# Kernel optimization log

Measured on AMD Instinct MI355X. Metric: run time of the kernel, lower is better.

## Reference

```python
import jax, jax.numpy as jnp
import numpy as np

B, H, S, DK = 2, 16, 2048, 64


def setup_inputs() -> dict:
    key = jax.random.key(0)
    k1, k2, k3, k4 = jax.random.split(key, 4)
    Q = jax.random.normal(k1, (B, H, S, DK), dtype=jnp.float32)
    K = jax.random.normal(k2, (B, H, S, DK), dtype=jnp.float32)
    V = jax.random.normal(k3, (B, H, S, DK), dtype=jnp.float32)
    attn_mask = jax.random.randint(k4, (B, 1, S, S), 0, 2).astype(jnp.bool_)
    return {"Q": Q, "K": K, "V": V, "attn_mask": attn_mask}


def reference(Q, K, V, attn_mask):
    d_k = Q.shape[-1]
    scale = 1.0 / jnp.sqrt(jnp.asarray(d_k, dtype=Q.dtype))
    # scores: [B,H,S,S]
    scores = jnp.einsum('bhqd,bhkd->bhqk', Q, K) * scale
    scores = jnp.where(attn_mask, jnp.asarray(-1e9, dtype=scores.dtype), scores)
    attn = jax.nn.softmax(scores, axis=-1)
    # dropout in eval mode (identity) for deterministic reference
    return jnp.einsum('bhqk,bhkd->bhqd', attn, V)
```

## Files before the change

### kernel.cpp

```cpp
#include <hip/hip_runtime.h>
#include <hip/hip_bf16.h>

#define Bdim 2
#define Hdim 16
#define Sdim 2048
#define Ddim 64
#define NT2 64
#define WQ 32
#define NWAVE 4
#define QTILE (WQ * NWAVE)
#define QSCL (0.125f * 1.44269504088896f)
#define SCALE 0.125f
#define WREG 8192

typedef __bf16 bf16x8 __attribute__((ext_vector_type(8)));
typedef float  f32x4  __attribute__((ext_vector_type(4)));
typedef float  f32x16 __attribute__((ext_vector_type(16)));
typedef unsigned u32x4 __attribute__((ext_vector_type(4)));

__device__ __forceinline__ void gll16(const __bf16* g, __bf16* l) {
  __builtin_amdgcn_global_load_lds(
      (const __attribute__((address_space(1))) void*)g,
      (__attribute__((address_space(3))) void*)l, 16, 0, 0);
}
__device__ __forceinline__ unsigned cvtpk_raw(float lo, float hi) {
  unsigned r;
  asm("v_cvt_pk_bf16_f32 %0, %1, %2" : "=v"(r) : "v"(lo), "v"(hi));
  return r;
}
template <bool SW>
__device__ __forceinline__ unsigned pko(float a, float b) {
  return SW ? cvtpk_raw(b, a) : cvtpk_raw(a, b);
}
__device__ __forceinline__ unsigned cvtpk(float a, float b, bool sw) {
  const float lo = sw ? b : a;
  const float hi = sw ? a : b;
  return cvtpk_raw(lo, hi);
}
template <bool SW>
__device__ __forceinline__ void packAll32(const float (&sv)[16],
                                          unsigned (&pw)[8]) {
#pragma unroll
  for (int ks = 0; ks < 2; ++ks) {
    const int rb = 8 * ks;
    pw[ks * 4 + 0] = pko<SW>(sv[rb + 0], sv[rb + 1]);
    pw[ks * 4 + 1] = pko<SW>(sv[rb + 2], sv[rb + 3]);
    pw[ks * 4 + 2] = pko<SW>(sv[rb + 4], sv[rb + 5]);
    pw[ks * 4 + 3] = pko<SW>(sv[rb + 6], sv[rb + 7]);
  }
}

__global__ __launch_bounds__(256) void prep_all(
    const void* __restrict__ mask, unsigned long long* __restrict__ packed,
    const float* __restrict__ K, const float* __restrict__ V,
    __bf16* __restrict__ Kb, __bf16* __restrict__ Vt) {
  __shared__ __bf16 tile[64][72];
  const int t = threadIdx.x;

  if (blockIdx.x < 512) {
    const int nwords = Bdim * Sdim * (Sdim / 64);
    const unsigned* m32 = (const unsigned*)mask;
    const unsigned char* m8 = (const unsigned char*)mask;
    int gid = blockIdx.x * 256 + t;
    int lane = gid & 63;
    int wid = gid >> 6;
    const int nwaves = 512 * 256 / 64;
    bool isBytes = __any(m32[lane] > 1u);
    for (int w = wid; w < nwords; w += nwaves) {
      int v = isBytes ? (int)m8[(size_t)w * 64 + lane]
                      : (int)m32[(size_t)w * 64 + lane];
      unsigned long long bal = __ballot(v != 0);
      if (lane == 0) packed[w] = bal;
    }
    return;
  }

  const int idx = blockIdx.x - 512;
  const int bh = idx >> 5, st = idx & 31;
  const int r = t >> 2, c0 = (t & 3) << 4;
  {
    const float* ks = K + ((size_t)bh * Sdim + st * 64 + r) * Ddim + c0;
    bf16x8 o0, o1;
#pragma unroll
    for (int j = 0; j < 8; ++j) o0[j] = (__bf16)ks[j];
#pragma unroll
    for (int j = 0; j < 8; ++j) o1[j] = (__bf16)ks[8 + j];
    __bf16* kd = Kb + ((size_t)bh * Sdim + st * 64 + r) * Ddim + c0;
    *(bf16x8*)kd = o0;
    *(bf16x8*)(kd + 8) = o1;
  }
  {
    const float* vs = V + ((size_t)bh * Sdim + st * 64 + r) * Ddim + c0;
#pragma unroll
    for (int j = 0; j < 16; ++j) tile[r][c0 + j] = (__bf16)vs[j];
  }
  __syncthreads();
  {
    const int d = t >> 2, s0 = (t & 3) << 4;
    __bf16 o[16];
#pragma unroll
    for (int j = 0; j < 16; ++j) o[j] = tile[s0 + j][d];
    __bf16* dst = Vt + ((size_t)bh * Ddim + d) * Sdim + st * 64 + s0;
    *(bf16x8*)dst = *(bf16x8*)&o[0];
    *(bf16x8*)(dst + 8) = *(bf16x8*)&o[8];
  }
}

__global__ __launch_bounds__(256, 2) void attn7(
    const float* __restrict__ Q, const __bf16* __restrict__ Kb,
    const __bf16* __restrict__ Vt,
    const unsigned long long* __restrict__ maskP, float* __restrict__ Out) {
  __shared__ alignas(16) __bf16 sm[NWAVE * WREG];

  const int tid = threadIdx.x;
  const int lane = tid & 63;
  const int w = tid >> 6;
  const int l31 = lane & 31;
  const int hi = lane >> 5;

  const int bid = blockIdx.x;
  const int bh = bid & 31;
  const int qt = bid >> 5;
  const int b = bh >> 4;
  const int qrow = qt * QTILE + w * WQ + l31;

  const __bf16* Kbase = Kb + (size_t)bh * Sdim * Ddim;
  const __bf16* Vbase = Vt + (size_t)bh * (size_t)Ddim * Sdim;
  const unsigned* mp32 =
      (const unsigned*)(maskP + ((size_t)b * Sdim + qrow) * (Sdim / 64));

  __bf16* smw = sm + w * WREG;

  const bool sw = (cvtpk_raw(0.0f, 1.0f) & 0xFFFFu) != 0u;

  bf16x8 qf[4];
  {
    const float* qs = Q + ((size_t)bh * Sdim + qrow) * Ddim;
#pragma unroll
    for (int step = 0; step < 4; ++step) {
      const int d0 = step * 16 + hi * 8;
      float4 a = *(const float4*)(qs + d0);
      float4 c = *(const float4*)(qs + d0 + 4);
      u32x4 f;
      f[0] = cvtpk(a.x * QSCL, a.y * QSCL, sw);
      f[1] = cvtpk(a.z * QSCL, a.w * QSCL, sw);
      f[2] = cvtpk(c.x * QSCL, c.y * QSCL, sw);
      f[3] = cvtpk(c.z * QSCL, c.w * QSCL, sw);
      qf[step] = __builtin_bit_cast(bf16x8, f);
    }
  }

  const int lr3 = lane >> 3;
  const int ksb = (lane & 7) ^ lr3;
  const int vbp = (lane & 7) ^ lr3;
  const int vd0 = 2 * lr3 + (vbp >> 2);
  const int vsc = vbp & 3;

  const __bf16* kpS = Kbase + (size_t)lr3 * Ddim + ksb * 8;
  const __bf16* vpS = Vbase + (size_t)vd0 * Sdim + vsc * 8;

  const __bf16* kf[4];
#pragma unroll
  for (int s = 0; s < 4; ++s)
    kf[s] = smw + l31 * 64 + (((s * 2 + hi) ^ (l31 & 7)) << 3);
  const __bf16* vfp[2][2];
#pragma unroll
  for (int half = 0; half < 2; ++half)
#pragma unroll
    for (int ks = 0; ks < 2; ++ks)
      vfp[half][ks] = smw + 2048 + half * 1024 + (l31 >> 1) * 64 +
                      ((((l31 & 1) * 4 + ks * 2 + hi) ^ ((l31 >> 1) & 7)) << 3);

  f32x16 otA = {0,0,0,0,0,0,0,0,0,0,0,0,0,0,0,0};
  f32x16 otB = {0,0,0,0,0,0,0,0,0,0,0,0,0,0,0,0};
  float lrow = 0.f;

  unsigned mw32 = mp32[0];
  const unsigned* mpp = mp32 + 1;
  {
    gll16(kpS, smw);
    gll16(kpS + 8 * Ddim, smw + 512);
    gll16(kpS + 16 * Ddim, smw + 1024);
    gll16(kpS + 24 * Ddim, smw + 1536);
    gll16(vpS, smw + 2048);
    gll16(vpS + 16 * Sdim, smw + 2560);
    gll16(vpS + 32 * Sdim, smw + 3072);
    gll16(vpS + 48 * Sdim, smw + 3584);
    kpS += 32 * Ddim;
    vpS += 32;
  }

  unsigned mwNext;

#define ITER2(BUFC, STBUF, LAST)                                               \
  do {                                                                         \
    if (!(LAST)) {                                                             \
      mwNext = *mpp++;                                                         \
      gll16(kpS, smw + (STBUF));                                               \
      gll16(kpS + 8 * Ddim, smw + (STBUF) + 512);                              \
      gll16(kpS + 16 * Ddim, smw + (STBUF) + 1024);                            \
      gll16(kpS + 24 * Ddim, smw + (STBUF) + 1536);                            \
      gll16(vpS, smw + (STBUF) + 2048);                                        \
      gll16(vpS + 16 * Sdim, smw + (STBUF) + 2560);                            \
      gll16(vpS + 32 * Sdim, smw + (STBUF) + 3072);                            \
      gll16(vpS + 48 * Sdim, smw + (STBUF) + 3584);                            \
      kpS += 32 * Ddim;                                                        \
      vpS += 32;                                                               \
       \
      asm volatile("s_waitcnt vmcnt(9)" ::: "memory");                         \
    } else {                                                                   \
      asm volatile("s_waitcnt vmcnt(0)" ::: "memory");                         \
    }                                                                          \
    __builtin_amdgcn_sched_barrier(0);                                         \
    f32x16 st = {0,0,0,0,0,0,0,0,0,0,0,0,0,0,0,0};                             \
    __builtin_amdgcn_s_setprio(1);                                             \
    st = __builtin_amdgcn_mfma_f32_32x32x16_bf16(                              \
        *(const bf16x8*)(kf[0] + (BUFC)), qf[0], st, 0, 0, 0);                 \
    st = __builtin_amdgcn_mfma_f32_32x32x16_bf16(                              \
        *(const bf16x8*)(kf[1] + (BUFC)), qf[1], st, 0, 0, 0);                 \
    st = __builtin_amdgcn_mfma_f32_32x32x16_bf16(                              \
        *(const bf16x8*)(kf[2] + (BUFC)), qf[2], st, 0, 0, 0);                 \
    st = __builtin_amdgcn_mfma_f32_32x32x16_bf16(                              \
        *(const bf16x8*)(kf[3] + (BUFC)), qf[3], st, 0, 0, 0);                 \
    __builtin_amdgcn_s_setprio(0);                                             \
    float sv[16];                                                              \
    const unsigned ws_ = mw32 >> (hi * 4);                                     \
    _Pragma("unroll") for (int r = 0; r < 16; ++r) {                           \
      const int cr = (r & 3) + 8 * (r >> 2);                                   \
      const float e0 = __builtin_amdgcn_exp2f(st[r]);                          \
      sv[r] = ((ws_ >> cr) & 1u) ? 0.f : e0;                                   \
    }                                                                          \
    {                                                                          \
      float s8_[8];                                                            \
      _Pragma("unroll") for (int j = 0; j < 8; ++j) s8_[j] = sv[j] + sv[j + 8];\
      lrow += ((s8_[0] + s8_[4]) + (s8_[1] + s8_[5])) +                        \
              ((s8_[2] + s8_[6]) + (s8_[3] + s8_[7]));                         \
    }                                                                          \
    unsigned pw[8];                                                            \
    if (!sw) packAll32<false>(sv, pw);                                         \
    else     packAll32<true>(sv, pw);                                          \
    bf16x8 pb[2];                                                              \
    _Pragma("unroll") for (int ks = 0; ks < 2; ++ks) {                         \
      const unsigned W0 = pw[ks * 4 + 0], W1 = pw[ks * 4 + 1];                 \
      const unsigned X0 = pw[ks * 4 + 2], X1 = pw[ks * 4 + 3];                 \
      const unsigned s1 = hi ? W0 : X0;                                        \
      const unsigned s2 = hi ? W1 : X1;                                        \
      const unsigned r1 = __shfl_xor(s1, 32, 64);                              \
      const unsigned r2 = __shfl_xor(s2, 32, 64);                              \
      u32x4 wv;                                                                \
      wv[0] = hi ? r1 : W0;                                                    \
      wv[1] = hi ? r2 : W1;                                                    \
      wv[2] = hi ? X0 : r1;                                                    \
      wv[3] = hi ? X1 : r2;                                                    \
      pb[ks] = __builtin_bit_cast(bf16x8, wv);                                 \
    }                                                                          \
    __builtin_amdgcn_s_setprio(1);                                             \
    otA = __builtin_amdgcn_mfma_f32_32x32x16_bf16(                             \
        *(const bf16x8*)(vfp[0][0] + (BUFC)), pb[0], otA, 0, 0, 0);            \
    otA = __builtin_amdgcn_mfma_f32_32x32x16_bf16(                             \
        *(const bf16x8*)(vfp[0][1] + (BUFC)), pb[1], otA, 0, 0, 0);            \
    otB = __builtin_amdgcn_mfma_f32_32x32x16_bf16(                             \
        *(const bf16x8*)(vfp[1][0] + (BUFC)), pb[0], otB, 0, 0, 0);            \
    otB = __builtin_amdgcn_mfma_f32_32x32x16_bf16(                             \
        *(const bf16x8*)(vfp[1][1] + (BUFC)), pb[1], otB, 0, 0, 0);            \
    __builtin_amdgcn_s_setprio(0);                                             \
    mw32 = mwNext;                                                             \
  } while (0)

#pragma unroll 1
  for (int g = 0; g < 31; ++g) {
    ITER2(0, 4096, false);
    ITER2(4096, 0, false);
  }
  ITER2(0, 4096, false);
  ITER2(4096, 0, true);
#undef ITER2

  lrow += __shfl_xor(lrow, 32, 64);
  const float inv = 1.f / (lrow + 1e-30f);
  float* orow = Out + ((size_t)bh * Sdim + qrow) * Ddim;
#pragma unroll
  for (int g = 0; g < 4; ++g) {
    const int d0 = 8 * g + 4 * hi;
    float4 va = {otA[4 * g] * inv, otA[4 * g + 1] * inv,
                 otA[4 * g + 2] * inv, otA[4 * g + 3] * inv};
    float4 vb = {otB[4 * g] * inv, otB[4 * g + 1] * inv,
                 otB[4 * g + 2] * inv, otB[4 * g + 3] * inv};
    *(float4*)(orow + d0) = va;
    *(float4*)(orow + 32 + d0) = vb;
  }
}

__global__ __launch_bounds__(256) void attn_fallback(
    const float* __restrict__ Q, const float* __restrict__ K,
    const float* __restrict__ V, const void* __restrict__ maskRaw,
    float* __restrict__ Out) {
  __shared__ alignas(16) __bf16 Kl[64 * Ddim];
  __shared__ alignas(16) __bf16 Vts[Ddim * 64];
  __shared__ alignas(16) __bf16 Pl[4][16 * 64];

  const int tid = threadIdx.x;
  const int lane = tid & 63;
  const int w = tid >> 6;
  const int lhi = lane >> 4;
  const int llo = lane & 15;

  const int qt = blockIdx.x;
  const int bh = blockIdx.y;
  const int b = bh >> 4;
  const int qbase = qt * 64;

  const float* Qp = Q + (size_t)bh * Sdim * Ddim;
  const float* Kp = K + (size_t)bh * Sdim * Ddim;
  const float* Vp = V + (size_t)bh * Sdim * Ddim;

  bool maskBytes = __any(((const unsigned*)maskRaw)[lane] > 1u);

  bf16x8 qf0, qf1;
  {
    const int qr = qbase + w * 16 + llo;
    const float* src = Qp + (size_t)qr * Ddim + lhi * 8;
#pragma unroll
    for (int i = 0; i < 8; ++i) qf0[i] = (__bf16)(src[i] * SCALE);
#pragma unroll
    for (int i = 0; i < 8; ++i) qf1[i] = (__bf16)(src[32 + i] * SCALE);
  }

  f32x4 acc[4] = {{0.f,0.f,0.f,0.f},{0.f,0.f,0.f,0.f},
                  {0.f,0.f,0.f,0.f},{0.f,0.f,0.f,0.f}};
  float mrow[4], lrw[4];
#pragma unroll
  for (int r = 0; r < 4; ++r) { mrow[r] = -3.0e38f; lrw[r] = 0.f; }

  for (int kt = 0; kt < Sdim / 64; ++kt) {
    __syncthreads();
    {
      int r = tid >> 2;
      int c0 = (tid & 3) << 4;
      const float* ks = Kp + (size_t)(kt * 64 + r) * Ddim + c0;
      const float* vs = Vp + (size_t)(kt * 64 + r) * Ddim + c0;
      float kv[16], vv[16];
#pragma unroll
      for (int j = 0; j < 4; ++j) {
        *(float4*)(&kv[j * 4]) = *(const float4*)(ks + j * 4);
        *(float4*)(&vv[j * 4]) = *(const float4*)(vs + j * 4);
      }
      const int swzK = (r & 7) << 3;
      bf16x8 k0v, k1v;
#pragma unroll
      for (int j = 0; j < 8; ++j) { k0v[j] = (__bf16)kv[j]; k1v[j] = (__bf16)kv[8 + j]; }
      *(bf16x8*)&Kl[r * 64 + (c0 ^ swzK)] = k0v;
      *(bf16x8*)&Kl[r * 64 + ((c0 + 8) ^ swzK)] = k1v;
#pragma unroll
      for (int j = 0; j < 16; ++j) {
        int d = c0 + j;
        Vts[d * 64 + (r ^ ((d & 7) << 3))] = (__bf16)vv[j];
      }
    }
    __syncthreads();

    float sv[4][4];
#pragma unroll
    for (int cb = 0; cb < 4; ++cb) {
      int krow = cb * 16 + llo;
      int swz = (krow & 7) << 3;
      bf16x8 kf0 = *(const bf16x8*)&Kl[krow * 64 + ((lhi * 8) ^ swz)];
      bf16x8 kf1 = *(const bf16x8*)&Kl[krow * 64 + ((32 + lhi * 8) ^ swz)];
      f32x4 s = {0.f, 0.f, 0.f, 0.f};
      s = __builtin_amdgcn_mfma_f32_16x16x32_bf16(qf0, kf0, s, 0, 0, 0);
      s = __builtin_amdgcn_mfma_f32_16x16x32_bf16(qf1, kf1, s, 0, 0, 0);
#pragma unroll
      for (int r = 0; r < 4; ++r) {
        size_t q = qbase + w * 16 + lhi * 4 + r;
        size_t k = (size_t)kt * 64 + cb * 16 + llo;
        size_t idx = ((size_t)b * Sdim + q) * Sdim + k;
        bool masked = maskBytes ? (((const unsigned char*)maskRaw)[idx] != 0)
                                : (((const int*)maskRaw)[idx] != 0);
        sv[cb][r] = masked ? -1e9f : s[r];
      }
    }

    float corr[4], tsum[4];
#pragma unroll
    for (int r = 0; r < 4; ++r) {
      float mx = fmaxf(fmaxf(sv[0][r], sv[1][r]), fmaxf(sv[2][r], sv[3][r]));
#pragma unroll
      for (int off = 1; off < 16; off <<= 1)
        mx = fmaxf(mx, __shfl_xor(mx, off, 64));
      float mnew = fmaxf(mrow[r], mx);
      corr[r] = __expf(mrow[r] - mnew);
      mrow[r] = mnew;
      tsum[r] = 0.f;
    }
#pragma unroll
    for (int cb = 0; cb < 4; ++cb) {
#pragma unroll
      for (int r = 0; r < 4; ++r) {
        float p = __expf(sv[cb][r] - mrow[r]);
        tsum[r] += p;
        int row = lhi * 4 + r;
        int col = cb * 16 + llo;
        Pl[w][row * 64 + (col ^ ((row & 7) << 3))] = (__bf16)p;
      }
    }
#pragma unroll
    for (int r = 0; r < 4; ++r) {
      float s = tsum[r];
#pragma unroll
      for (int off = 1; off < 16; off <<= 1)
        s += __shfl_xor(s, off, 64);
      lrw[r] = lrw[r] * corr[r] + s;
#pragma unroll
      for (int db = 0; db < 4; ++db) acc[db][r] *= corr[r];
    }
    asm volatile("s_waitcnt lgkmcnt(0)" ::: "memory");

    bf16x8 pf0 = *(const bf16x8*)&Pl[w][llo * 64 + ((lhi * 8) ^ ((llo & 7) << 3))];
    bf16x8 pf1 = *(const bf16x8*)&Pl[w][llo * 64 + ((32 + lhi * 8) ^ ((llo & 7) << 3))];
#pragma unroll
    for (int db = 0; db < 4; ++db) {
      int d = db * 16 + llo;
      int swz = (d & 7) << 3;
      bf16x8 vf0 = *(const bf16x8*)&Vts[d * 64 + ((lhi * 8) ^ swz)];
      bf16x8 vf1 = *(const bf16x8*)&Vts[d * 64 + ((32 + lhi * 8) ^ swz)];
      acc[db] = __builtin_amdgcn_mfma_f32_16x16x32_bf16(pf0, vf0, acc[db], 0, 0, 0);
      acc[db] = __builtin_amdgcn_mfma_f32_16x16x32_bf16(pf1, vf1, acc[db], 0, 0, 0);
    }
  }

#pragma unroll
  for (int r = 0; r < 4; ++r) {
    float inv = 1.f / lrw[r];
    int q = qbase + w * 16 + lhi * 4 + r;
    float* dst = Out + ((size_t)bh * Sdim + q) * Ddim + llo;
#pragma unroll
    for (int db = 0; db < 4; ++db) dst[db * 16] = acc[db][r] * inv;
  }
}

extern "C" void kernel_launch(void* const* d_in, const int* in_sizes, int n_in,
                              void* d_out, int out_size, void* d_ws, size_t ws_size,
                              hipStream_t stream) {
  const float* Q = (const float*)d_in[0];
  const float* K = (const float*)d_in[1];
  const float* V = (const float*)d_in[2];
  const void* mask = d_in[3];
  float* out = (float*)d_out;

  const size_t packed_bytes =
      (size_t)Bdim * Sdim * (Sdim / 64) * sizeof(unsigned long long);
  const size_t tensor_bf16 = (size_t)Bdim * Hdim * Sdim * Ddim * 2;

  if (ws_size >= packed_bytes + 2 * tensor_bf16) {
    unsigned long long* packed = (unsigned long long*)d_ws;
    __bf16* Kb = (__bf16*)((char*)d_ws + packed_bytes);
    __bf16* Vt = (__bf16*)((char*)d_ws + packed_bytes + tensor_bf16);
    prep_all<<<512 + Bdim * Hdim * (Sdim / 64), 256, 0, stream>>>(
        mask, packed, K, V, Kb, Vt);
    attn7<<<(Sdim / QTILE) * Bdim * Hdim, 256, 0, stream>>>(Q, Kb, Vt, packed, out);
  } else {
    attn_fallback<<<dim3(Sdim / 64, Bdim * Hdim), 256, 0, stream>>>(Q, K, V, mask, out);
  }
}
```

Baseline: 111.3 us.

## Share K/V tiles across waves with triple-buffered LDS and two interleaved KV halves

Before, each wave loaded its own private copy of every K/V tile into LDS. Now all four waves cooperatively stage one shared K/V tile per step into a triple-buffered LDS ring, synchronised with a block barrier, which cuts global-to-LDS traffic by about four times. The key sequence is split into two halves that are processed in the same loop iteration, giving two independent QK^T/softmax/PV chains for more instruction-level parallelism. It also swaps the shuffle-based P repacking for v_permlane32_swap, whose operand order is detected at runtime, and uses a bitmask AND in place of a select when applying the mask. The trade-off is a block-wide barrier every step and higher register pressure from the two chains.

```diff
diff --git a/kernel.cpp b/kernel.cpp
--- a/kernel.cpp
+++ b/kernel.cpp
@@ -5,13 +5,15 @@
 #define Hdim 16
 #define Sdim 2048
 #define Ddim 64
-#define NT2 64
+#define NTH 32
 #define WQ 32
 #define NWAVE 4
 #define QTILE (WQ * NWAVE)
 #define QSCL (0.125f * 1.44269504088896f)
 #define SCALE 0.125f
-#define WREG 8192
+#define TBE 4096
+#define TVOFF 2048
+#define BOFF_B 12288
 
 typedef __bf16 bf16x8 __attribute__((ext_vector_type(8)));
 typedef float  f32x4  __attribute__((ext_vector_type(4)));
@@ -37,17 +39,8 @@
   const float hi = sw ? a : b;
   return cvtpk_raw(lo, hi);
 }
-template <bool SW>
-__device__ __forceinline__ void packAll32(const float (&sv)[16],
-                                          unsigned (&pw)[8]) {
-#pragma unroll
-  for (int ks = 0; ks < 2; ++ks) {
-    const int rb = 8 * ks;
-    pw[ks * 4 + 0] = pko<SW>(sv[rb + 0], sv[rb + 1]);
-    pw[ks * 4 + 1] = pko<SW>(sv[rb + 2], sv[rb + 3]);
-    pw[ks * 4 + 2] = pko<SW>(sv[rb + 4], sv[rb + 5]);
-    pw[ks * 4 + 3] = pko<SW>(sv[rb + 6], sv[rb + 7]);
-  }
+__device__ __forceinline__ void pswap(unsigned& a, unsigned& b) {
+  asm volatile("v_permlane32_swap_b32 %0, %1" : "+v"(a), "+v"(b));
 }
 
 __global__ __launch_bounds__(256) void prep_all(
@@ -106,17 +99,18 @@
   }
 }
 
-__global__ __launch_bounds__(256, 2) void attn7(
+__global__ __launch_bounds__(256, 2) void attn10(
     const float* __restrict__ Q, const __bf16* __restrict__ Kb,
     const __bf16* __restrict__ Vt,
     const unsigned long long* __restrict__ maskP, float* __restrict__ Out) {
-  __shared__ alignas(16) __bf16 sm[NWAVE * WREG];
+  __shared__ alignas(16) __bf16 sm[6 * TBE];
 
   const int tid = threadIdx.x;
   const int lane = tid & 63;
   const int w = tid >> 6;
   const int l31 = lane & 31;
   const int hi = lane >> 5;
+  const int lr3 = lane >> 3;
 
   const int bid = blockIdx.x;
   const int bh = bid & 31;
@@ -129,9 +123,14 @@
   const unsigned* mp32 =
       (const unsigned*)(maskP + ((size_t)b * Sdim + qrow) * (Sdim / 64));
 
-  __bf16* smw = sm + w * WREG;
-
   const bool sw = (cvtpk_raw(0.0f, 1.0f) & 0xFFFFu) != 0u;
+  bool semA;
+  {
+    unsigned p0 = hi ? 222u : 111u;
+    unsigned p1 = hi ? 444u : 333u;
+    pswap(p0, p1);
+    semA = __any(hi && (p0 == 333u));
+  }
 
   bf16x8 qf[4];
   {
@@ -150,85 +149,55 @@
     }
   }
 
-  const int lr3 = lane >> 3;
-  const int ksb = (lane & 7) ^ lr3;
-  const int vbp = (lane & 7) ^ lr3;
-  const int vd0 = 2 * lr3 + (vbp >> 2);
+  const int srow = 8 * w + lr3;
+  const int sblk = (lane & 7) ^ (lr3 & 7);
+  const int vbp = (lane & 7) ^ (lr3 & 7);
+  const int vd0 = (vbp >> 2);
   const int vsc = vbp & 3;
-
-  const __bf16* kpS = Kbase + (size_t)lr3 * Ddim + ksb * 8;
-  const __bf16* vpS = Vbase + (size_t)vd0 * Sdim + vsc * 8;
-
-  const __bf16* kf[4];
+  const int dstw = w * 512;
+
+  const __bf16* kA = Kbase + (size_t)srow * Ddim + sblk * 8;
+  const __bf16* kB = kA + (size_t)1024 * Ddim;
+  const __bf16* vA = Vbase + (size_t)(2 * (8 * w + lr3) + vd0) * Sdim + vsc * 8;
+  const __bf16* vB = vA + 1024;
+
+#define STAGE(base_, kp_, vp_, kt_)                                         \
+  do {                                                                      \
+    gll16((kp_) + (size_t)(kt_) * 32 * Ddim, &sm[(base_) + dstw]);          \
+    gll16((vp_) + (size_t)(kt_) * 32, &sm[(base_) + TVOFF + dstw]);         \
+  } while (0)
+
+  int kfo[4];
 #pragma unroll
   for (int s = 0; s < 4; ++s)
-    kf[s] = smw + l31 * 64 + (((s * 2 + hi) ^ (l31 & 7)) << 3);
-  const __bf16* vfp[2][2];
+    kfo[s] = l31 * 64 + (((s * 2 + hi) ^ (l31 & 7)) << 3);
+  int vfo[2][2];
 #pragma unroll
   for (int half = 0; half < 2; ++half)
 #pragma unroll
     for (int ks = 0; ks < 2; ++ks)
-      vfp[half][ks] = smw + 2048 + half * 1024 + (l31 >> 1) * 64 +
+      vfo[half][ks] = TVOFF + half * 1024 + (l31 >> 1) * 64 +
                       ((((l31 & 1) * 4 + ks * 2 + hi) ^ ((l31 >> 1) & 7)) << 3);
 
-  f32x16 otA = {0,0,0,0,0,0,0,0,0,0,0,0,0,0,0,0};
-  f32x16 otB = {0,0,0,0,0,0,0,0,0,0,0,0,0,0,0,0};
-  float lrow = 0.f;
-
-  unsigned mw32 = mp32[0];
-  const unsigned* mpp = mp32 + 1;
-  {
-    gll16(kpS, smw);
-    gll16(kpS + 8 * Ddim, smw + 512);
-    gll16(kpS + 16 * Ddim, smw + 1024);
-    gll16(kpS + 24 * Ddim, smw + 1536);
-    gll16(vpS, smw + 2048);
-    gll16(vpS + 16 * Sdim, smw + 2560);
-    gll16(vpS + 32 * Sdim, smw + 3072);
-    gll16(vpS + 48 * Sdim, smw + 3584);
-    kpS += 32 * Ddim;
-    vpS += 32;
-  }
-
-  unsigned mwNext;
-
-#define ITER2(BUFC, STBUF, LAST)                                               \
+#define QKT32(OFF, d)                                                          \
   do {                                                                         \
-    if (!(LAST)) {                                                             \
-      mwNext = *mpp++;                                                         \
-      gll16(kpS, smw + (STBUF));                                               \
-      gll16(kpS + 8 * Ddim, smw + (STBUF) + 512);                              \
-      gll16(kpS + 16 * Ddim, smw + (STBUF) + 1024);                            \
-      gll16(kpS + 24 * Ddim, smw + (STBUF) + 1536);                            \
-      gll16(vpS, smw + (STBUF) + 2048);                                        \
-      gll16(vpS + 16 * Sdim, smw + (STBUF) + 2560);                            \
-      gll16(vpS + 32 * Sdim, smw + (STBUF) + 3072);                            \
-      gll16(vpS + 48 * Sdim, smw + (STBUF) + 3584);                            \
-      kpS += 32 * Ddim;                                                        \
-      vpS += 32;                                                               \
-       \
-      asm volatile("s_waitcnt vmcnt(9)" ::: "memory");                         \
-    } else {                                                                   \
-      asm volatile("s_waitcnt vmcnt(0)" ::: "memory");                         \
-    }                                                                          \
-    __builtin_amdgcn_sched_barrier(0);                                         \
-    f32x16 st = {0,0,0,0,0,0,0,0,0,0,0,0,0,0,0,0};                             \
     __builtin_amdgcn_s_setprio(1);                                             \
-    st = __builtin_amdgcn_mfma_f32_32x32x16_bf16(                              \
-        *(const bf16x8*)(kf[0] + (BUFC)), qf[0], st, 0, 0, 0);                 \
-    st = __builtin_amdgcn_mfma_f32_32x32x16_bf16(                              \
-        *(const bf16x8*)(kf[1] + (BUFC)), qf[1], st, 0, 0, 0);                 \
-    st = __builtin_amdgcn_mfma_f32_32x32x16_bf16(                              \
-        *(const bf16x8*)(kf[2] + (BUFC)), qf[2], st, 0, 0, 0);                 \
-    st = __builtin_amdgcn_mfma_f32_32x32x16_bf16(                              \
-        *(const bf16x8*)(kf[3] + (BUFC)), qf[3], st, 0, 0, 0);                 \
+    _Pragma("unroll") for (int step = 0; step < 4; ++step) {                   \
+      bf16x8 kf = *(const bf16x8*)&sm[(OFF) + kfo[step]];                      \
+      d = __builtin_amdgcn_mfma_f32_32x32x16_bf16(kf, qf[step], d, 0, 0, 0);   \
+    }                                                                          \
     __builtin_amdgcn_s_setprio(0);                                             \
+  } while (0)
+
+#define SMPV32(st_, MW, OFF)                                                   \
+  do {                                                                         \
     float sv[16];                                                              \
-    const unsigned ws_ = mw32 >> (hi * 4);                                     \
+    const unsigned ws_ = (~(MW)) >> (hi * 4);                                  \
     _Pragma("unroll") for (int r = 0; r < 16; ++r) {                           \
       const int cr = (r & 3) + 8 * (r >> 2);                                   \
-      const float e0 = __builtin_amdgcn_exp2f(st[r]);                          \
-      sv[r] = ((ws_ >> cr) & 1u) ? 0.f : e0;                                   \
+      const float e0 = __builtin_amdgcn_exp2f(st_[r]);                         \
+      const int k0 = ((int)(ws_ << (31 - cr))) >> 31;                          \
+      sv[r] = __builtin_bit_cast(float, __builtin_bit_cast(int, e0) & k0);     \
     }                                                                          \
     {                                                                          \
       float s8_[8];                                                            \
@@ -237,44 +206,82 @@
               ((s8_[2] + s8_[6]) + (s8_[3] + s8_[7]));                         \
     }                                                                          \
     unsigned pw[8];                                                            \
-    if (!sw) packAll32<false>(sv, pw);                                         \
-    else     packAll32<true>(sv, pw);                                          \
+    _Pragma("unroll") for (int ks = 0; ks < 2; ++ks) {                         \
+      const int rb = 8 * ks;                                                   \
+      if (!sw) {                                                               \
+        pw[ks * 4 + 0] = pko<false>(sv[rb + 0], sv[rb + 1]);                   \
+        pw[ks * 4 + 1] = pko<false>(sv[rb + 2], sv[rb + 3]);                   \
+        pw[ks * 4 + 2] = pko<false>(sv[rb + 4], sv[rb + 5]);                   \
+        pw[ks * 4 + 3] = pko<false>(sv[rb + 6], sv[rb + 7]);                   \
+      } else {                                                                 \
+        pw[ks * 4 + 0] = pko<true>(sv[rb + 0], sv[rb + 1]);                    \
+        pw[ks * 4 + 1] = pko<true>(sv[rb + 2], sv[rb + 3]);                    \
+        pw[ks * 4 + 2] = pko<true>(sv[rb + 4], sv[rb + 5]);                    \
+        pw[ks * 4 + 3] = pko<true>(sv[rb + 6], sv[rb + 7]);                    \
+      }                                                                        \
+    }                                                                          \
     bf16x8 pb[2];                                                              \
     _Pragma("unroll") for (int ks = 0; ks < 2; ++ks) {                         \
-      const unsigned W0 = pw[ks * 4 + 0], W1 = pw[ks * 4 + 1];                 \
-      const unsigned X0 = pw[ks * 4 + 2], X1 = pw[ks * 4 + 3];                 \
-      const unsigned s1 = hi ? W0 : X0;                                        \
-      const unsigned s2 = hi ? W1 : X1;                                        \
-      const unsigned r1 = __shfl_xor(s1, 32, 64);                              \
-      const unsigned r2 = __shfl_xor(s2, 32, 64);                              \
+      unsigned W0 = pw[ks * 4 + 0], W1 = pw[ks * 4 + 1];                       \
+      unsigned X0 = pw[ks * 4 + 2], X1 = pw[ks * 4 + 3];                       \
+      if (semA) { pswap(W0, X0); pswap(W1, X1); }                              \
+      else      { pswap(X0, W0); pswap(X1, W1); }                              \
       u32x4 wv;                                                                \
-      wv[0] = hi ? r1 : W0;                                                    \
-      wv[1] = hi ? r2 : W1;                                                    \
-      wv[2] = hi ? X0 : r1;                                                    \
-      wv[3] = hi ? X1 : r2;                                                    \
+      wv[0] = W0; wv[1] = W1; wv[2] = X0; wv[3] = X1;                          \
       pb[ks] = __builtin_bit_cast(bf16x8, wv);                                 \
     }                                                                          \
     __builtin_amdgcn_s_setprio(1);                                             \
-    otA = __builtin_amdgcn_mfma_f32_32x32x16_bf16(                             \
-        *(const bf16x8*)(vfp[0][0] + (BUFC)), pb[0], otA, 0, 0, 0);            \
-    otA = __builtin_amdgcn_mfma_f32_32x32x16_bf16(                             \
-        *(const bf16x8*)(vfp[0][1] + (BUFC)), pb[1], otA, 0, 0, 0);            \
-    otB = __builtin_amdgcn_mfma_f32_32x32x16_bf16(                             \
-        *(const bf16x8*)(vfp[1][0] + (BUFC)), pb[0], otB, 0, 0, 0);            \
-    otB = __builtin_amdgcn_mfma_f32_32x32x16_bf16(                             \
-        *(const bf16x8*)(vfp[1][1] + (BUFC)), pb[1], otB, 0, 0, 0);            \
+    _Pragma("unroll") for (int ks = 0; ks < 2; ++ks) {                         \
+      bf16x8 vf0 = *(const bf16x8*)&sm[(OFF) + vfo[0][ks]];                    \
+      otA = __builtin_amdgcn_mfma_f32_32x32x16_bf16(vf0, pb[ks], otA, 0, 0, 0);\
+      bf16x8 vf1 = *(const bf16x8*)&sm[(OFF) + vfo[1][ks]];                    \
+      otB = __builtin_amdgcn_mfma_f32_32x32x16_bf16(vf1, pb[ks], otB, 0, 0, 0);\
+    }                                                                          \
     __builtin_amdgcn_s_setprio(0);                                             \
-    mw32 = mwNext;                                                             \
   } while (0)
 
+  f32x16 otA = {0,0,0,0,0,0,0,0,0,0,0,0,0,0,0,0};
+  f32x16 otB = {0,0,0,0,0,0,0,0,0,0,0,0,0,0,0,0};
+  float lrow = 0.f;
+
+  unsigned mwA = mp32[0], mwB = mp32[32];
+  unsigned mwAn, mwBn;
+  STAGE(0, kA, vA, 0);
+  STAGE(BOFF_B, kB, vB, 0);
+  int rdA = 0, stA_ = TBE;
+  int rdB = BOFF_B, stB_ = BOFF_B + TBE;
+
 #pragma unroll 1
-  for (int g = 0; g < 31; ++g) {
-    ITER2(0, 4096, false);
-    ITER2(4096, 0, false);
-  }
-  ITER2(0, 4096, false);
-  ITER2(4096, 0, true);
-#undef ITER2
+  for (int t = 0; t < NTH; ++t) {
+    if (t + 1 < NTH) {
+      mwAn = mp32[t + 1];
+      mwBn = mp32[32 + t + 1];
+      STAGE(stA_, kA, vA, t + 1);
+      STAGE(stB_, kB, vB, t + 1);
+      asm volatile("s_waitcnt vmcnt(6)" ::: "memory");
+    } else {
+      asm volatile("s_waitcnt vmcnt(0)" ::: "memory");
+    }
+    __builtin_amdgcn_s_barrier();
+    __builtin_amdgcn_sched_barrier(0);
+
+    f32x16 stVA = {0,0,0,0,0,0,0,0,0,0,0,0,0,0,0,0};
+    f32x16 stVB = {0,0,0,0,0,0,0,0,0,0,0,0,0,0,0,0};
+    QKT32(rdA, stVA);
+    QKT32(rdB, stVB);
+    SMPV32(stVA, mwA, rdA);
+    SMPV32(stVB, mwB, rdB);
+
+    mwA = mwAn;
+    mwB = mwBn;
+    rdA = stA_;
+    stA_ = (stA_ == 2 * TBE) ? 0 : stA_ + TBE;
+    rdB = stB_;
+    stB_ = (stB_ == BOFF_B + 2 * TBE) ? BOFF_B : stB_ + TBE;
+  }
+#undef SMPV32
+#undef QKT32
+#undef STAGE
 
   lrow += __shfl_xor(lrow, 32, 64);
   const float inv = 1.f / (lrow + 1e-30f);
@@ -457,7 +464,7 @@
     __bf16* Vt = (__bf16*)((char*)d_ws + packed_bytes + tensor_bf16);
     prep_all<<<512 + Bdim * Hdim * (Sdim / 64), 256, 0, stream>>>(
         mask, packed, K, V, Kb, Vt);
-    attn7<<<(Sdim / QTILE) * Bdim * Hdim, 256, 0, stream>>>(Q, Kb, Vt, packed, out);
+    attn10<<<(Sdim / QTILE) * Bdim * Hdim, 256, 0, stream>>>(Q, Kb, Vt, packed, out);
   } else {
     attn_fallback<<<dim3(Sdim / 64, Bdim * Hdim), 256, 0, stream>>>(Q, K, V, mask, out);
   }
```

New measurement: 102.5 us. 7.9% less time.
